# Kernel tuning notes

Measured on AMD Instinct MI355X. Metric: run time of the kernel, lower is better.

Reference implementation:

```python
import jax, jax.numpy as jnp
import numpy as np

NUM_HEADS = 12

def setup_inputs() -> dict:
    key = jax.random.key(0)
    ks = jax.random.split(key, 4)
    B, N, C = 64, 512, 768
    x = jax.random.normal(ks[0], (B, N, C), dtype=jnp.float32)
    qkv_w = jax.random.normal(ks[1], (3 * C, C), dtype=jnp.float32) * 0.02
    proj_w = jax.random.normal(ks[2], (C, C), dtype=jnp.float32) * 0.02
    proj_b = jnp.zeros((C,), dtype=jnp.float32)
    bias_table = jax.random.normal(ks[3], (2 * N - 1, NUM_HEADS), dtype=jnp.float32) * 0.02
    return {"x": x, "qkv_w": qkv_w, "proj_w": proj_w, "proj_b": proj_b, "bias_table": bias_table}

def reference(x, qkv_w, proj_w, proj_b, bias_table):
    B, N, C = x.shape
    H = NUM_HEADS
    hd = C // H
    scale = hd ** (-0.5)
    # qkv projection (no bias): [B,N,3C] -> [3,B,H,N,hd]
    qkv = (x @ qkv_w.T).reshape(B, N, 3, H, hd)
    qkv = jnp.transpose(qkv, (2, 0, 3, 1, 4))
    q, k, v = qkv[0], qkv[1], qkv[2]
    # relative position bias: rel index in [0, 2N-2]
    coords = jnp.arange(N)
    rel = coords[:, None] - coords[None, :] + (N - 1)  # [N,N]
    bias = jnp.transpose(bias_table[rel], (2, 0, 1))   # [H,N,N]
    attn = jnp.einsum('bhnd,bhmd->bhnm', q, k) * scale + bias[None]
    attn = jax.nn.softmax(attn, axis=-1)
    out = jnp.einsum('bhnm,bhmd->bhnd', attn, v)       # [B,H,N,hd]
    out = jnp.transpose(out, (0, 2, 1, 3)).reshape(B, N, C)
    return out @ proj_w.T + proj_b
```

## Files before the change

### kernel.cpp

```cpp
#include <hip/hip_runtime.h>
#include <hip/hip_bf16.h>

#define DI static __device__ __forceinline__

typedef __attribute__((ext_vector_type(8), may_alias)) short short8;
typedef __attribute__((ext_vector_type(4), may_alias)) short short4a;
typedef __attribute__((ext_vector_type(4), may_alias)) float floatx4a;
typedef __attribute__((ext_vector_type(4))) float floatx4;

constexpr int Bsz = 64, Nseq = 512, Cdim = 768, NH = 12, HD = 64;
constexpr int QS = Bsz * NH * Nseq * HD;
constexpr float QK_PRESCALE = 0.18033688011112042f;
constexpr float LOG2E = 1.4426950408889634f;

DI ushort f2bf(float f) {
  union { float f; unsigned u; } v; v.f = f;
  unsigned r = v.u + 0x7FFF + ((v.u >> 16) & 1);
  return (ushort)(r >> 16);
}
DI float bf2f(ushort u) {
  union { unsigned u; float f; } v; v.u = ((unsigned)u) << 16;
  return v.f;
}

DI void gload_lds16(const ushort* g, ushort* l) {
  __builtin_amdgcn_global_load_lds(
      (const __attribute__((address_space(1))) unsigned int*)g,
      (__attribute__((address_space(3))) unsigned int*)l, 16, 0, 0);
}

__global__ void cvt8(const float* __restrict__ s, ushort* __restrict__ d, int n) {
  int i = (blockIdx.x * 256 + threadIdx.x) * 8;
  if (i >= n) return;
  floatx4a a = *(const floatx4a*)(s + i);
  floatx4a b = *(const floatx4a*)(s + i + 4);
  short8 r;
  r[0] = (short)f2bf(a[0]); r[1] = (short)f2bf(a[1]);
  r[2] = (short)f2bf(a[2]); r[3] = (short)f2bf(a[3]);
  r[4] = (short)f2bf(b[0]); r[5] = (short)f2bf(b[1]);
  r[6] = (short)f2bf(b[2]); r[7] = (short)f2bf(b[3]);
  *(short8*)(d + i) = r;
}
__global__ void cvt1s(const float* __restrict__ s, ushort* __restrict__ d, int n) {
  int i = blockIdx.x * 256 + threadIdx.x;
  if (i < n) d[i] = f2bf(s[i] * LOG2E);
}

__global__ __launch_bounds__(512, 2) void qkv_gemm(
    const ushort* __restrict__ x, const ushort* __restrict__ w,
    ushort* __restrict__ qo, ushort* __restrict__ ko, ushort* __restrict__ vo)
{
  __shared__ __align__(16) ushort As[2][256 * 64];
  __shared__ __align__(16) ushort Ws[2][256 * 64];
  const int id = blockIdx.y * 9 + blockIdx.x;
  const int swz = (id & 7) * 144 + (id >> 3);
  const int bm = swz / 9;
  const int bn = swz % 9;
  const int t = threadIdx.x;
  const int wv = t >> 6, ln = t & 63, lq = ln >> 4, lm = ln & 15;
  const int wm = wv >> 2, wn = wv & 3;

  const int srow = ln >> 3;
  const int scol = (((ln & 7) ^ srow) << 3);
  const int cswz = (lm & 7) << 3;

  floatx4 acc[8][4];
  #pragma unroll
  for (int i = 0; i < 8; ++i)
    #pragma unroll
    for (int j = 0; j < 4; ++j) acc[i][j] = (floatx4)0.f;

  auto stage = [&](int buf, int kt) {
    #pragma unroll
    for (int p = 0; p < 4; ++p) {
      int c = wv * 4 + p;
      int row = c * 8 + srow;
      gload_lds16(&x[(size_t)(bm * 256 + row) * Cdim + kt * 64 + scol],
                  &As[buf][c * 512]);
      gload_lds16(&w[(size_t)(bn * 256 + row) * Cdim + kt * 64 + scol],
                  &Ws[buf][c * 512]);
    }
  };

  stage(0, 0);
  for (int kt = 0; kt < 12; ++kt) {
    const int cur = kt & 1;
    if (kt < 11) {
      stage(cur ^ 1, kt + 1);
      asm volatile("s_waitcnt vmcnt(8)" ::: "memory");
    } else {
      asm volatile("s_waitcnt vmcnt(0)" ::: "memory");
    }
    __builtin_amdgcn_s_barrier();
    #pragma unroll
    for (int ks = 0; ks < 2; ++ks) {
      short8 af[8], bfr[4];
      #pragma unroll
      for (int i = 0; i < 8; ++i)
        af[i] = *(const short8*)&As[cur][(wm * 128 + i * 16 + lm) * 64 +
                                         ((ks * 32 + lq * 8) ^ cswz)];
      #pragma unroll
      for (int j = 0; j < 4; ++j)
        bfr[j] = *(const short8*)&Ws[cur][(wn * 64 + j * 16 + lm) * 64 +
                                          ((ks * 32 + lq * 8) ^ cswz)];
      #pragma unroll
      for (int i = 0; i < 8; ++i)
        #pragma unroll
        for (int j = 0; j < 4; ++j)
          acc[i][j] = __builtin_amdgcn_mfma_f32_16x16x32_bf16(af[i], bfr[j], acc[i][j], 0, 0, 0);
    }
    asm volatile("s_waitcnt lgkmcnt(0)" ::: "memory");
    __builtin_amdgcn_s_barrier();
  }

  const int cbase = bn * 256 + wn * 64;
  const int which = cbase / Cdim;
  const int h = (cbase % Cdim) >> 6;
  const float osc = (which == 0) ? QK_PRESCALE : 1.f;
  #pragma unroll
  for (int i = 0; i < 8; ++i) {
    int gm0 = bm * 256 + wm * 128 + i * 16 + lq * 4;
    int b = gm0 >> 9, ns0 = gm0 & 511;
    #pragma unroll
    for (int j = 0; j < 4; ++j) {
      int d = j * 16 + lm;
      if (which == 2) {
        short4a v4;
        #pragma unroll
        for (int r = 0; r < 4; ++r) v4[r] = (short)f2bf(acc[i][j][r]);
        *(short4a*)&vo[(size_t)((b * NH + h) * HD + d) * Nseq + ns0] = v4;
      } else {
        ushort* outp = which == 0 ? qo : ko;
        #pragma unroll
        for (int r = 0; r < 4; ++r)
          outp[(size_t)((b * NH + h) * Nseq + ns0 + r) * HD + d] = f2bf(acc[i][j][r] * osc);
      }
    }
  }
}

__global__ __launch_bounds__(256) void attn_kernel(
    const ushort* __restrict__ q, const ushort* __restrict__ k,
    const ushort* __restrict__ vt, const ushort* __restrict__ bt,
    ushort* __restrict__ ao)
{
  __shared__ __align__(16) ushort Ks[64 * 72];
  __shared__ __align__(16) ushort Vs[64 * 72];
  __shared__ __align__(16) ushort Ps[64 * 72];
  __shared__ float biasAll[8][128];
  const int blk = blockIdx.x;
  const int xcd = blk & 7;
  const int slot = blk >> 3;
  const int qt = slot & 7;
  const int bh = xcd * 96 + (slot >> 3);
  const int h = bh % NH, b = bh / NH;
  const int t = threadIdx.x;
  const int wv = t >> 6, ln = t & 63, lq = ln >> 4, lm = ln & 15;
  const size_t base = (size_t)bh * (Nseq * HD);

  short8 qa[2];
  #pragma unroll
  for (int ks = 0; ks < 2; ++ks)
    qa[ks] = *(const short8*)&q[base + (size_t)(qt * 64 + wv * 16 + lm) * HD +
                                ks * 32 + lq * 8];

  if (t < 127) {
    #pragma unroll
    for (int kt2 = 0; kt2 < 8; ++kt2)
      biasAll[kt2][t] = bf2f(bt[(qt * 64 - kt2 * 64 + 448 + t) * NH + h]);
  }

  floatx4 o[4];
  #pragma unroll
  for (int i = 0; i < 4; ++i) o[i] = (floatx4)0.f;
  float lrow[4];
  #pragma unroll
  for (int r = 0; r < 4; ++r) lrow[r] = 0.f;

  for (int kt = 0; kt < Nseq / 64; ++kt) {
    #pragma unroll
    for (int i = 0; i < 2; ++i) {
      int id = t + 256 * i;
      int r = id >> 3, c = (id & 7) << 3;
      *(short8*)&Ks[r * 72 + c] =
          *(const short8*)&k[base + (size_t)(kt * 64 + r) * HD + c];
      *(short8*)&Vs[r * 72 + c] =
          *(const short8*)&vt[base + (size_t)r * Nseq + kt * 64 + c];
    }
    __syncthreads();

    floatx4 s[4];
    #pragma unroll
    for (int cb = 0; cb < 4; ++cb) s[cb] = (floatx4)0.f;
    #pragma unroll
    for (int ks = 0; ks < 2; ++ks) {
      #pragma unroll
      for (int cb = 0; cb < 4; ++cb) {
        short8 bfr = *(const short8*)&Ks[(cb * 16 + lm) * 72 + ks * 32 + lq * 8];
        s[cb] = __builtin_amdgcn_mfma_f32_16x16x32_bf16(qa[ks], bfr, s[cb], 0, 0, 0);
      }
    }

    #pragma unroll
    for (int r = 0; r < 4; ++r) {
      int row_in = wv * 16 + lq * 4 + r;
      #pragma unroll
      for (int cb = 0; cb < 4; ++cb) {
        int col_in = cb * 16 + lm;
        float p = __builtin_amdgcn_exp2f(s[cb][r] + biasAll[kt][row_in - col_in + 63]);
        lrow[r] += p;
        Ps[row_in * 72 + col_in] = f2bf(p);
      }
    }

    #pragma unroll
    for (int ks = 0; ks < 2; ++ks) {
      short8 a = *(const short8*)&Ps[(wv * 16 + lm) * 72 + ks * 32 + lq * 8];
      #pragma unroll
      for (int db = 0; db < 4; ++db) {
        short8 bfr = *(const short8*)&Vs[(db * 16 + lm) * 72 + ks * 32 + lq * 8];
        o[db] = __builtin_amdgcn_mfma_f32_16x16x32_bf16(a, bfr, o[db], 0, 0, 0);
      }
    }
    __syncthreads();
  }

  #pragma unroll
  for (int r = 0; r < 4; ++r) {
    #pragma unroll
    for (int off = 8; off; off >>= 1) lrow[r] += __shfl_xor(lrow[r], off);
  }

  #pragma unroll
  for (int r = 0; r < 4; ++r) {
    int qi = qt * 64 + wv * 16 + lq * 4 + r;
    float inv = 1.f / lrow[r];
    #pragma unroll
    for (int db = 0; db < 4; ++db) {
      int d = db * 16 + lm;
      ao[(size_t)(b * Nseq + qi) * Cdim + h * HD + d] = f2bf(o[db][r] * inv);
    }
  }
}

__global__ __launch_bounds__(256, 2) void proj_gemm(
    const ushort* __restrict__ a, const ushort* __restrict__ w,
    const ushort* __restrict__ pb, float* __restrict__ out)
{
  __shared__ __align__(16) ushort As[2][128 * 64];
  __shared__ __align__(16) ushort Ws[2][128 * 64];
  const int id = blockIdx.y * 6 + blockIdx.x;
  const int swz = (id & 7) * 192 + (id >> 3);
  const int bm = swz / 6;
  const int bn = swz % 6;
  const int t = threadIdx.x;
  const int wv = t >> 6, ln = t & 63, lq = ln >> 4, lm = ln & 15;
  const int wm = wv >> 1, wn = wv & 1;

  const int srow = ln >> 3;
  const int scol = (((ln & 7) ^ srow) << 3);
  const int cswz = (lm & 7) << 3;

  floatx4 acc[4][4];
  #pragma unroll
  for (int i = 0; i < 4; ++i)
    #pragma unroll
    for (int j = 0; j < 4; ++j) acc[i][j] = (floatx4)0.f;

  auto stage = [&](int buf, int kt) {
    #pragma unroll
    for (int p = 0; p < 4; ++p) {
      int c = wv * 4 + p;
      int row = c * 8 + srow;
      gload_lds16(&a[(size_t)(bm * 128 + row) * Cdim + kt * 64 + scol],
                  &As[buf][c * 512]);
      gload_lds16(&w[(size_t)(bn * 128 + row) * Cdim + kt * 64 + scol],
                  &Ws[buf][c * 512]);
    }
  };

  stage(0, 0);
  for (int kt = 0; kt < 12; ++kt) {
    const int cur = kt & 1;
    if (kt < 11) {
      stage(cur ^ 1, kt + 1);
      asm volatile("s_waitcnt vmcnt(8)" ::: "memory");
    } else {
      asm volatile("s_waitcnt vmcnt(0)" ::: "memory");
    }
    __builtin_amdgcn_s_barrier();
    #pragma unroll
    for (int ks = 0; ks < 2; ++ks) {
      short8 af[4], bfr[4];
      #pragma unroll
      for (int i = 0; i < 4; ++i)
        af[i] = *(const short8*)&As[cur][(wm * 64 + i * 16 + lm) * 64 +
                                         ((ks * 32 + lq * 8) ^ cswz)];
      #pragma unroll
      for (int j = 0; j < 4; ++j)
        bfr[j] = *(const short8*)&Ws[cur][(wn * 64 + j * 16 + lm) * 64 +
                                          ((ks * 32 + lq * 8) ^ cswz)];
      #pragma unroll
      for (int i = 0; i < 4; ++i)
        #pragma unroll
        for (int j = 0; j < 4; ++j)
          acc[i][j] = __builtin_amdgcn_mfma_f32_16x16x32_bf16(af[i], bfr[j], acc[i][j], 0, 0, 0);
    }
    asm volatile("s_waitcnt lgkmcnt(0)" ::: "memory");
    __builtin_amdgcn_s_barrier();
  }

  #pragma unroll
  for (int j = 0; j < 4; ++j) {
    int gn = bn * 128 + wn * 64 + j * 16 + lm;
    float bias = bf2f(pb[gn]);
    #pragma unroll
    for (int i = 0; i < 4; ++i) {
      #pragma unroll
      for (int r = 0; r < 4; ++r) {
        int gm = bm * 128 + wm * 64 + i * 16 + lq * 4 + r;
        out[(size_t)gm * Cdim + gn] = acc[i][j][r] + bias;
      }
    }
  }
}

extern "C" void kernel_launch(void* const* d_in, const int* in_sizes, int n_in,
                              void* d_out, int out_size, void* d_ws, size_t ws_size,
                              hipStream_t stream) {
  const float* x  = (const float*)d_in[0];
  const float* qw = (const float*)d_in[1];
  const float* pw = (const float*)d_in[2];
  const float* pb = (const float*)d_in[3];
  const float* bt = (const float*)d_in[4];
  float* out = (float*)d_out;

  constexpr int NX = Bsz * Nseq * Cdim;
  constexpr int NQW = 3 * Cdim * Cdim;
  constexpr int NPW = Cdim * Cdim;
  constexpr int NBT = (2 * Nseq - 1) * NH;

  ushort* qs  = (ushort*)d_ws;
  ushort* ks  = qs + QS;
  ushort* vts = ks + QS;
  ushort* ao  = vts + QS;
  ushort* xb  = ao;
  ushort* qwb = ao + QS;
  ushort* pwb = qwb + NQW;
  ushort* pbb = pwb + NPW;
  ushort* btb = pbb + Cdim;

  cvt8<<<(NX  + 2047) / 2048, 256, 0, stream>>>(x,  xb,  NX);
  cvt8<<<(NQW + 2047) / 2048, 256, 0, stream>>>(qw, qwb, NQW);
  cvt8<<<(NPW + 2047) / 2048, 256, 0, stream>>>(pw, pwb, NPW);
  cvt8<<<1, 256, 0, stream>>>(pb, pbb, Cdim);
  cvt1s<<<(NBT + 255) / 256, 256, 0, stream>>>(bt, btb, NBT);

  qkv_gemm<<<dim3(9, 128), 512, 0, stream>>>(xb, qwb, qs, ks, vts);
  attn_kernel<<<dim3(Bsz * NH * (Nseq / 64)), 256, 0, stream>>>(qs, ks, vts, btb, ao);
  proj_gemm<<<dim3(6, 256), 256, 0, stream>>>(ao, pwb, pbb, out);
}
```

Measured before the change: 500.9 us.

## Process two query tiles per attention block to reuse staged K/V tiles

Each attention block now handles two 64-row query tiles, not one, so the grid is halved. Every K and V tile staged into shared memory is used by both query tiles, which halves global K/V traffic and the number of barriers per query. The per-block bias table becomes a single 640-entry strip indexed by relative offset. The cost is roughly double the accumulator and Q-fragment registers and half as many blocks, which may lower occupancy and latency hiding.

```diff
diff --git a/kernel.cpp b/kernel.cpp
--- a/kernel.cpp
+++ b/kernel.cpp
@@ -147,35 +147,35 @@
   __shared__ __align__(16) ushort Ks[64 * 72];
   __shared__ __align__(16) ushort Vs[64 * 72];
   __shared__ __align__(16) ushort Ps[64 * 72];
-  __shared__ float biasAll[8][128];
+  __shared__ float biasStrip[640];
   const int blk = blockIdx.x;
   const int xcd = blk & 7;
   const int slot = blk >> 3;
-  const int qt = slot & 7;
-  const int bh = xcd * 96 + (slot >> 3);
+  const int qp = slot & 3;
+  const int bh = xcd * 96 + (slot >> 2);
   const int h = bh % NH, b = bh / NH;
   const int t = threadIdx.x;
   const int wv = t >> 6, ln = t & 63, lq = ln >> 4, lm = ln & 15;
   const size_t base = (size_t)bh * (Nseq * HD);
-
-  short8 qa[2];
-  #pragma unroll
-  for (int ks = 0; ks < 2; ++ks)
-    qa[ks] = *(const short8*)&q[base + (size_t)(qt * 64 + wv * 16 + lm) * HD +
-                                ks * 32 + lq * 8];
-
-  if (t < 127) {
-    #pragma unroll
-    for (int kt2 = 0; kt2 < 8; ++kt2)
-      biasAll[kt2][t] = bf2f(bt[(qt * 64 - kt2 * 64 + 448 + t) * NH + h]);
-  }
-
-  floatx4 o[4];
-  #pragma unroll
-  for (int i = 0; i < 4; ++i) o[i] = (floatx4)0.f;
-  float lrow[4];
-  #pragma unroll
-  for (int r = 0; r < 4; ++r) lrow[r] = 0.f;
+  const int qt0 = qp * 2;
+
+  short8 qa[2][2];
+  #pragma unroll
+  for (int j = 0; j < 2; ++j)
+    #pragma unroll
+    for (int ks = 0; ks < 2; ++ks)
+      qa[j][ks] = *(const short8*)&q[base +
+          (size_t)((qt0 + j) * 64 + wv * 16 + lm) * HD + ks * 32 + lq * 8];
+
+  for (int j = t; j < 640; j += 256)
+    biasStrip[j] = bf2f(bt[(qt0 * 64 + j) * NH + h]);
+
+  floatx4 o[2][4];
+  float lrow[2][4];
+  #pragma unroll
+  for (int j = 0; j < 2; ++j)
+    #pragma unroll
+    for (int i = 0; i < 4; ++i) { o[j][i] = (floatx4)0.f; lrow[j][i] = 0.f; }
 
   for (int kt = 0; kt < Nseq / 64; ++kt) {
     #pragma unroll
@@ -189,56 +189,63 @@
     }
     __syncthreads();
 
-    floatx4 s[4];
-    #pragma unroll
-    for (int cb = 0; cb < 4; ++cb) s[cb] = (floatx4)0.f;
-    #pragma unroll
-    for (int ks = 0; ks < 2; ++ks) {
-      #pragma unroll
-      for (int cb = 0; cb < 4; ++cb) {
-        short8 bfr = *(const short8*)&Ks[(cb * 16 + lm) * 72 + ks * 32 + lq * 8];
-        s[cb] = __builtin_amdgcn_mfma_f32_16x16x32_bf16(qa[ks], bfr, s[cb], 0, 0, 0);
-      }
-    }
-
+    #pragma unroll
+    for (int j = 0; j < 2; ++j) {
+      floatx4 s[4];
+      #pragma unroll
+      for (int cb = 0; cb < 4; ++cb) s[cb] = (floatx4)0.f;
+      #pragma unroll
+      for (int ks = 0; ks < 2; ++ks) {
+        #pragma unroll
+        for (int cb = 0; cb < 4; ++cb) {
+          short8 bfr = *(const short8*)&Ks[(cb * 16 + lm) * 72 + ks * 32 + lq * 8];
+          s[cb] = __builtin_amdgcn_mfma_f32_16x16x32_bf16(qa[j][ks], bfr, s[cb], 0, 0, 0);
+        }
+      }
+
+      const int bbase = j * 64 - kt * 64 + 511;
+      #pragma unroll
+      for (int r = 0; r < 4; ++r) {
+        int row_in = wv * 16 + lq * 4 + r;
+        #pragma unroll
+        for (int cb = 0; cb < 4; ++cb) {
+          int col_in = cb * 16 + lm;
+          float p = __builtin_amdgcn_exp2f(s[cb][r] +
+                                           biasStrip[bbase + row_in - col_in]);
+          lrow[j][r] += p;
+          Ps[row_in * 72 + col_in] = f2bf(p);
+        }
+      }
+
+      #pragma unroll
+      for (int ks = 0; ks < 2; ++ks) {
+        short8 a = *(const short8*)&Ps[(wv * 16 + lm) * 72 + ks * 32 + lq * 8];
+        #pragma unroll
+        for (int db = 0; db < 4; ++db) {
+          short8 bfr = *(const short8*)&Vs[(db * 16 + lm) * 72 + ks * 32 + lq * 8];
+          o[j][db] = __builtin_amdgcn_mfma_f32_16x16x32_bf16(a, bfr, o[j][db], 0, 0, 0);
+        }
+      }
+    }
+    __syncthreads();
+  }
+
+  #pragma unroll
+  for (int j = 0; j < 2; ++j) {
     #pragma unroll
     for (int r = 0; r < 4; ++r) {
-      int row_in = wv * 16 + lq * 4 + r;
-      #pragma unroll
-      for (int cb = 0; cb < 4; ++cb) {
-        int col_in = cb * 16 + lm;
-        float p = __builtin_amdgcn_exp2f(s[cb][r] + biasAll[kt][row_in - col_in + 63]);
-        lrow[r] += p;
-        Ps[row_in * 72 + col_in] = f2bf(p);
-      }
-    }
-
-    #pragma unroll
-    for (int ks = 0; ks < 2; ++ks) {
-      short8 a = *(const short8*)&Ps[(wv * 16 + lm) * 72 + ks * 32 + lq * 8];
+      #pragma unroll
+      for (int off = 8; off; off >>= 1) lrow[j][r] += __shfl_xor(lrow[j][r], off);
+    }
+    #pragma unroll
+    for (int r = 0; r < 4; ++r) {
+      int qi = (qt0 + j) * 64 + wv * 16 + lq * 4 + r;
+      float inv = 1.f / lrow[j][r];
       #pragma unroll
       for (int db = 0; db < 4; ++db) {
-        short8 bfr = *(const short8*)&Vs[(db * 16 + lm) * 72 + ks * 32 + lq * 8];
-        o[db] = __builtin_amdgcn_mfma_f32_16x16x32_bf16(a, bfr, o[db], 0, 0, 0);
-      }
-    }
-    __syncthreads();
-  }
-
-  #pragma unroll
-  for (int r = 0; r < 4; ++r) {
-    #pragma unroll
-    for (int off = 8; off; off >>= 1) lrow[r] += __shfl_xor(lrow[r], off);
-  }
-
-  #pragma unroll
-  for (int r = 0; r < 4; ++r) {
-    int qi = qt * 64 + wv * 16 + lq * 4 + r;
-    float inv = 1.f / lrow[r];
-    #pragma unroll
-    for (int db = 0; db < 4; ++db) {
-      int d = db * 16 + lm;
-      ao[(size_t)(b * Nseq + qi) * Cdim + h * HD + d] = f2bf(o[db][r] * inv);
+        int d = db * 16 + lm;
+        ao[(size_t)(b * Nseq + qi) * Cdim + h * HD + d] = f2bf(o[j][db][r] * inv);
+      }
     }
   }
 }
@@ -357,6 +364,6 @@
   cvt1s<<<(NBT + 255) / 256, 256, 0, stream>>>(bt, btb, NBT);
 
   qkv_gemm<<<dim3(9, 128), 512, 0, stream>>>(xb, qwb, qs, ks, vts);
-  attn_kernel<<<dim3(Bsz * NH * (Nseq / 64)), 256, 0, stream>>>(qs, ks, vts, btb, ao);
+  attn_kernel<<<dim3(Bsz * NH * (Nseq / 128)), 256, 0, stream>>>(qs, ks, vts, btb, ao);
   proj_gemm<<<dim3(6, 256), 256, 0, stream>>>(ao, pwb, pbb, out);
 }
```

After: 502.3 us. Within noise of the previous version (+0.3%).
